# Kernel optimization log

Measured on AMD Instinct MI355X. Metric: run time of the kernel, lower is better.

The kernel has to match this reference:

```python
import jax, jax.numpy as jnp
import numpy as np

B, C, D, H = 2, 512, 512, 8
DH = D // H  # d_head = 64


def setup_inputs() -> dict:
    key = jax.random.key(0)
    ks = jax.random.split(key, 8)
    init = lambda k, shape: 0.02 * jax.random.normal(k, shape, dtype=jnp.float32)
    return {
        "x": jax.random.normal(ks[0], (B, C, D), dtype=jnp.float32),
        "Wq": init(ks[1], (D, D)), "bq": jnp.zeros((D,), jnp.float32),
        "Wk": init(ks[2], (D, D)), "bk": jnp.zeros((D,), jnp.float32),
        "Wv": init(ks[3], (D, D)), "bv": jnp.zeros((D,), jnp.float32),
        "W1": init(ks[4], (3 * DH, DH)), "b1": jnp.zeros((DH,), jnp.float32),
        "W2": init(ks[5], (DH, 1)), "b2": jnp.zeros((1,), jnp.float32),
        "Wo": init(ks[6], (D, D)), "bo": jnp.zeros((D,), jnp.float32),
    }


def reference(x, Wq, bq, Wk, bk, Wv, bv, W1, b1, W2, b2, Wo, bo):
    b, c, dm = x.shape
    # projections -> [B, H, C, d_head]
    q = (x @ Wq + bq).reshape(b, c, H, DH).transpose(0, 2, 1, 3)
    k = (x @ Wk + bk).reshape(b, c, H, DH).transpose(0, 2, 1, 3)
    v = (x @ Wv + bv).reshape(b, c, H, DH).transpose(0, 2, 1, 3)
    # split first MLP weight: [q || k || q*k] @ W1 = q@W1q + k@W1k + (q*k)@W1i
    W1q, W1k, W1i = W1[:DH], W1[DH:2 * DH], W1[2 * DH:]
    hq = jnp.einsum('bhid,de->bhie', q, W1q)   # [B,H,C,d]
    hk = jnp.einsum('bhjd,de->bhje', k, W1k)   # [B,H,C,d]
    hi = jnp.einsum('bhid,bhjd,de->bhije', q, k, W1i)  # [B,H,C,C,d] dominant intermediate
    h = hi + hq[:, :, :, None, :] + hk[:, :, None, :, :] + b1
    g = jax.nn.gelu(h, approximate=False)  # torch nn.GELU is exact erf form
    scores = (jnp.einsum('bhije,e->bhij', g, W2[:, 0]) + b2[0]) / (DH ** 0.5)
    attn = jax.nn.softmax(scores, axis=-1)  # dropout is identity in eval
    out = jnp.einsum('bhij,bhjd->bhid', attn, v)
    out = out.transpose(0, 2, 1, 3).reshape(b, c, dm)
    return out @ Wo + bo
```

## Files before the change

kernel.cpp:

```cpp
#include <hip/hip_runtime.h>
#include <hip/hip_bf16.h>
#include <math.h>

#define BB 2
#define CC 512
#define DD 512
#define HH 8
#define DH 64
#define TI 8

typedef __attribute__((ext_vector_type(8))) short short8;
typedef __attribute__((ext_vector_type(16))) float floatx16;
typedef __attribute__((ext_vector_type(2))) float float2v;
typedef unsigned short u16;

__device__ __forceinline__ float fast_rcp(float x) {
#if __has_builtin(__builtin_amdgcn_rcpf)
    return __builtin_amdgcn_rcpf(x);
#else
    return 1.0f / x;
#endif
}

__device__ __forceinline__ unsigned pk_bf16(float a, float b) {
    __hip_bfloat162 h2 = __float22bfloat162_rn(make_float2(a, b));
    unsigned r;
    __builtin_memcpy(&r, &h2, 4);
    return r;
}

__device__ __forceinline__ short8 mk_short8(unsigned u0, unsigned u1,
                                            unsigned u2, unsigned u3) {
    uint4 u = make_uint4(u0, u1, u2, u3);
    short8 r;
    __builtin_memcpy(&r, &u, 16);
    return r;
}

__device__ __forceinline__ float2v pkfma(float2v a, float2v b, float2v c) {
#if __has_builtin(__builtin_elementwise_fma)
    return __builtin_elementwise_fma(a, b, c);
#else
    float2v r; r[0] = fmaf(a[0], b[0], c[0]); r[1] = fmaf(a[1], b[1], c[1]);
    return r;
#endif
}

__device__ __forceinline__ void split_pack(const float* src, unsigned* hpk, unsigned* lpk) {
    #pragma unroll
    for (int p = 0; p < 4; ++p) {
        float a = src[2 * p], b = src[2 * p + 1];
        unsigned hp = pk_bf16(a, b);
        float la = a - __uint_as_float(hp << 16);
        float lb = b - __uint_as_float(hp & 0xffff0000u);
        hpk[p] = hp;
        lpk[p] = pk_bf16(la, lb);
    }
}

#define GC0 0.3989422804f
#define GC1 (-0.0664903801f)

__device__ __forceinline__ float2v gelu_dot2(float2v h, float2v w2, float2v p) {
    float2v s = h * h;
    float2v q = pkfma(s, float2v{GC1, GC1}, float2v{GC0, GC0});
    float2v t = s * q;
    float2v g = pkfma(h, float2v{0.5f, 0.5f}, t);
    return pkfma(g, w2, p);
}

__global__ __launch_bounds__(256) void prep(
    const float* __restrict__ Wq, const float* __restrict__ Wk,
    const float* __restrict__ Wv, const float* __restrict__ Wo,
    const float* __restrict__ W1, const float* __restrict__ b1,
    const float* __restrict__ bq,
    u16* __restrict__ wth, u16* __restrict__ wtl,
    u16* __restrict__ woh, u16* __restrict__ wol,
    float* __restrict__ b1p)
{
    __shared__ float SH[3 * 64 * 68];
    int j = blockIdx.x, t = threadIdx.x;
    if (j < 256) {
        int mat = j >> 6;
        const float* W = (mat == 0) ? Wq : (mat == 1) ? Wk : (mat == 2) ? Wv : Wo;
        u16* oh = (mat < 3) ? wth + (size_t)mat * 262144 : woh;
        u16* ol = (mat < 3) ? wtl + (size_t)mat * 262144 : wol;
        int tile = j & 63;
        int k0 = (tile >> 3) * 64, n0 = (tile & 7) * 64;
        float (*TT)[68] = (float(*)[68])SH;
        int r = t >> 4, c4 = (t & 15) * 4;
        #pragma unroll
        for (int rr = 0; rr < 4; ++rr) {
            int k = r + rr * 16;
            float4 v = *(const float4*)&W[(size_t)(k0 + k) * 512 + n0 + c4];
            TT[c4 + 0][k] = v.x; TT[c4 + 1][k] = v.y;
            TT[c4 + 2][k] = v.z; TT[c4 + 3][k] = v.w;
        }
        __syncthreads();
        int n = t >> 2, kc = (t & 3) * 16;
        #pragma unroll
        for (int g = 0; g < 2; ++g) {
            unsigned hpk[4], lpk[4];
            split_pack(&TT[n][kc + g * 8], hpk, lpk);
            *(uint4*)&oh[(size_t)(n0 + n) * 512 + k0 + kc + g * 8] =
                make_uint4(hpk[0], hpk[1], hpk[2], hpk[3]);
            *(uint4*)&ol[(size_t)(n0 + n) * 512 + k0 + kc + g * 8] =
                make_uint4(lpk[0], lpk[1], lpk[2], lpk[3]);
        }
    } else if (j < 320) {
        int jj = j - 256;
        int D0 = (jj >> 3) * 64, h = jj & 7;
        float (*WQ)[68]  = (float(*)[68])SH;
        float (*W1Q)[68] = (float(*)[68])(SH + 64 * 68);
        float (*OT)[68]  = (float(*)[68])(SH + 2 * 64 * 68);
        int r = t >> 4, c4 = (t & 15) * 4;
        #pragma unroll
        for (int rr = 0; rr < 4; ++rr) {
            int d = r + rr * 16;
            *(float4*)&WQ[d][c4]  = *(const float4*)&Wq[(size_t)(D0 + d) * 512 + h * 64 + c4];
            *(float4*)&W1Q[d][c4] = *(const float4*)&W1[(size_t)d * 64 + c4];
        }
        __syncthreads();
        int D = t & 63, ec = (t >> 6) * 16;
        float outv[16];
        #pragma unroll
        for (int i = 0; i < 16; ++i) outv[i] = 0.0f;
        for (int d4 = 0; d4 < 16; ++d4) {
            float4 wq4 = *(float4*)&WQ[D][d4 * 4];
            float wqa[4] = {wq4.x, wq4.y, wq4.z, wq4.w};
            #pragma unroll
            for (int dd = 0; dd < 4; ++dd) {
                float wv_ = wqa[dd];
                const float* wrow = &W1Q[d4 * 4 + dd][ec];
                #pragma unroll
                for (int i = 0; i < 16; ++i) outv[i] = fmaf(wv_, wrow[i], outv[i]);
            }
        }
        #pragma unroll
        for (int i = 0; i < 16; ++i) OT[ec + i][D] = outv[i];
        __syncthreads();
        int n = t >> 2, kc = (t & 3) * 16;
        u16* oh3 = wth + (size_t)3 * 262144;
        u16* ol3 = wtl + (size_t)3 * 262144;
        #pragma unroll
        for (int g = 0; g < 2; ++g) {
            unsigned hpk[4], lpk[4];
            split_pack(&OT[n][kc + g * 8], hpk, lpk);
            *(uint4*)&oh3[(size_t)(h * 64 + n) * 512 + D0 + kc + g * 8] =
                make_uint4(hpk[0], hpk[1], hpk[2], hpk[3]);
            *(uint4*)&ol3[(size_t)(h * 64 + n) * 512 + D0 + kc + g * 8] =
                make_uint4(lpk[0], lpk[1], lpk[2], lpk[3]);
        }
    } else {
        for (int n = t; n < 512; n += 256) {
            int h = n >> 6, e = n & 63;
            float s = b1[e];
            for (int d = 0; d < 64; ++d)
                s = fmaf(bq[h * 64 + d], W1[(size_t)d * 64 + e], s);
            b1p[n] = s;
        }
    }
}

__global__ __launch_bounds__(256) void gemm_qkv(
    const float* __restrict__ x,
    const u16* __restrict__ wth, const u16* __restrict__ wtl,
    const float* __restrict__ bq, const float* __restrict__ bk,
    const float* __restrict__ bv, const float* __restrict__ b1p,
    float* __restrict__ qw, float* __restrict__ kw, float* __restrict__ vw,
    float* __restrict__ hqc)
{
    __shared__ u16 Ah[64][64], Al[64][64], Bh[64][64], Bl[64][64];
    int t = threadIdx.x;
    int m0 = blockIdx.x * 64;
    int ny = blockIdx.y;
    int mat = ny >> 3, n0 = (ny & 7) * 64;
    const u16* WH = wth + (size_t)mat * 262144;
    const u16* WL = wtl + (size_t)mat * 262144;
    const float* bias = (mat == 0) ? bq : (mat == 1) ? bk : (mat == 2) ? bv : b1p;
    float* out = (mat == 0) ? qw : (mat == 1) ? kw : (mat == 2) ? vw : hqc;

    int lane = t & 63, w = t >> 6;
    int mrow = (w & 1) * 32, ncol = (w >> 1) * 32;
    int col = lane & 31, half = lane >> 5;
    int sr = t >> 2, skc = (t & 3) * 16;

    floatx16 acc = {0.0f,0.0f,0.0f,0.0f,0.0f,0.0f,0.0f,0.0f,
                    0.0f,0.0f,0.0f,0.0f,0.0f,0.0f,0.0f,0.0f};

    for (int k0 = 0; k0 < 512; k0 += 64) {
        float xa[16];
        const float* xr = &x[(size_t)(m0 + sr) * 512 + k0 + skc];
        *(float4*)&xa[0]  = *(const float4*)&xr[0];
        *(float4*)&xa[4]  = *(const float4*)&xr[4];
        *(float4*)&xa[8]  = *(const float4*)&xr[8];
        *(float4*)&xa[12] = *(const float4*)&xr[12];
        #pragma unroll
        for (int g = 0; g < 2; ++g) {
            unsigned hpk[4], lpk[4];
            split_pack(&xa[g * 8], hpk, lpk);
            int gg = (skc >> 3) + g;
            int sw = (gg ^ (sr & 7)) * 8;
            *(uint4*)&Ah[sr][sw] = make_uint4(hpk[0], hpk[1], hpk[2], hpk[3]);
            *(uint4*)&Al[sr][sw] = make_uint4(lpk[0], lpk[1], lpk[2], lpk[3]);
            *(uint4*)&Bh[sr][sw] = *(const uint4*)&WH[(size_t)(n0 + sr) * 512 + k0 + skc + g * 8];
            *(uint4*)&Bl[sr][sw] = *(const uint4*)&WL[(size_t)(n0 + sr) * 512 + k0 + skc + g * 8];
        }
        __syncthreads();
        int ar = mrow + col, br = ncol + col;
        #pragma unroll
        for (int kk = 0; kk < 4; ++kk) {
            int g8 = kk * 2 + half;
            short8 ah = *(short8*)&Ah[ar][(g8 ^ (ar & 7)) * 8];
            short8 al = *(short8*)&Al[ar][(g8 ^ (ar & 7)) * 8];
            short8 bh = *(short8*)&Bh[br][(g8 ^ (br & 7)) * 8];
            short8 bl = *(short8*)&Bl[br][(g8 ^ (br & 7)) * 8];
            acc = __builtin_amdgcn_mfma_f32_32x32x16_bf16(al, bh, acc, 0, 0, 0);
            acc = __builtin_amdgcn_mfma_f32_32x32x16_bf16(ah, bl, acc, 0, 0, 0);
            acc = __builtin_amdgcn_mfma_f32_32x32x16_bf16(ah, bh, acc, 0, 0, 0);
        }
        __syncthreads();
    }
    int h = n0 >> 6;
    int e = ncol + col;
    float bv_ = bias[n0 + e];
    #pragma unroll
    for (int reg = 0; reg < 16; ++reg) {
        int r = m0 + mrow + (reg & 3) + 8 * (reg >> 2) + 4 * half;
        int b = r >> 9, c = r & 511;
        out[((size_t)(b * HH + h) * CC + c) * DH + e] = acc[reg] + bv_;
    }
}

__global__ __launch_bounds__(256) void gemm_out(
    const float* __restrict__ ow,
    const u16* __restrict__ woh, const u16* __restrict__ wol,
    const float* __restrict__ bo, float* __restrict__ y)
{
    __shared__ u16 Ah[64][64], Al[64][64], Bh[64][64], Bl[64][64];
    int t = threadIdx.x;
    int m0 = blockIdx.x * 64, n0 = blockIdx.y * 64;
    int lane = t & 63, w = t >> 6;
    int mrow = (w & 1) * 32, ncol = (w >> 1) * 32;
    int col = lane & 31, half = lane >> 5;
    int sr = t >> 2, skc = (t & 3) * 16;

    floatx16 acc = {0.0f,0.0f,0.0f,0.0f,0.0f,0.0f,0.0f,0.0f,
                    0.0f,0.0f,0.0f,0.0f,0.0f,0.0f,0.0f,0.0f};
    int r = m0 + sr, b = r >> 9, c = r & 511;

    for (int k0 = 0; k0 < 512; k0 += 64) {
        int hh = k0 >> 6;
        float xa[16];
        const float* arow = &ow[((size_t)(b * HH + hh) * CC + c) * DH + skc];
        *(float4*)&xa[0]  = *(const float4*)&arow[0];
        *(float4*)&xa[4]  = *(const float4*)&arow[4];
        *(float4*)&xa[8]  = *(const float4*)&arow[8];
        *(float4*)&xa[12] = *(const float4*)&arow[12];
        #pragma unroll
        for (int g = 0; g < 2; ++g) {
            unsigned hpk[4], lpk[4];
            split_pack(&xa[g * 8], hpk, lpk);
            int gg = (skc >> 3) + g;
            int sw = (gg ^ (sr & 7)) * 8;
            *(uint4*)&Ah[sr][sw] = make_uint4(hpk[0], hpk[1], hpk[2], hpk[3]);
            *(uint4*)&Al[sr][sw] = make_uint4(lpk[0], lpk[1], lpk[2], lpk[3]);
            *(uint4*)&Bh[sr][sw] = *(const uint4*)&woh[(size_t)(n0 + sr) * 512 + k0 + skc + g * 8];
            *(uint4*)&Bl[sr][sw] = *(const uint4*)&wol[(size_t)(n0 + sr) * 512 + k0 + skc + g * 8];
        }
        __syncthreads();
        int ar = mrow + col, br = ncol + col;
        #pragma unroll
        for (int kk = 0; kk < 4; ++kk) {
            int g8 = kk * 2 + half;
            short8 ah = *(short8*)&Ah[ar][(g8 ^ (ar & 7)) * 8];
            short8 al = *(short8*)&Al[ar][(g8 ^ (ar & 7)) * 8];
            short8 bh = *(short8*)&Bh[br][(g8 ^ (br & 7)) * 8];
            short8 bl = *(short8*)&Bl[br][(g8 ^ (br & 7)) * 8];
            acc = __builtin_amdgcn_mfma_f32_32x32x16_bf16(al, bh, acc, 0, 0, 0);
            acc = __builtin_amdgcn_mfma_f32_32x32x16_bf16(ah, bl, acc, 0, 0, 0);
            acc = __builtin_amdgcn_mfma_f32_32x32x16_bf16(ah, bh, acc, 0, 0, 0);
        }
        __syncthreads();
    }
    float bv_ = bo[n0 + ncol + col];
    #pragma unroll
    for (int reg = 0; reg < 16; ++reg) {
        int r2 = m0 + mrow + (reg & 3) + 8 * (reg >> 2) + 4 * half;
        y[(size_t)r2 * 512 + n0 + ncol + col] = acc[reg] + bv_;
    }
}

__global__ __launch_bounds__(256, 2) void attn2(
    const float* qw, const float* __restrict__ kw,
    const float* __restrict__ vw, const float* __restrict__ hqc,
    const float* __restrict__ W1, const float* __restrict__ W2,
    const float* __restrict__ b2p,
    float* ow)
{
    __shared__ u16 Alds[2][64][64];
    __shared__ u16 sc16[TI][512];

    int t = threadIdx.x;
    int lane = t & 63;
    int w = t >> 6;
    int h = lane >> 5;
    int col = lane & 31;

    int bid = blockIdx.x;
    int bh = ((bid & 7) << 1) | (bid >> 9);
    int i0 = ((bid >> 3) & 63) * TI;

    const float* qb  = qw  + ((size_t)bh * CC + i0) * DH;
    const float* hb  = hqc + ((size_t)bh * CC + i0) * DH;
    const float* kb  = kw  + (size_t)bh * CC * DH;
    const float* vb  = vw  + (size_t)bh * CC * DH;

    float w1i_r[16], w1k_r[16];
    {
        int dbase = w * 16;
        #pragma unroll
        for (int dd = 0; dd < 16; ++dd) {
            w1i_r[dd] = W1[(size_t)(128 + dbase + dd) * 64 + lane];
            w1k_r[dd] = W1[(size_t)(64 + dbase + dd) * 64 + lane];
        }
    }

    short8 bfrag[4][4];
    for (int n = 0; n < 4; ++n) {
        int j = w * 128 + n * 32 + col;
        const float* kr = kb + (size_t)j * 64;
        #pragma unroll
        for (int kk = 0; kk < 4; ++kk) {
            int d = kk * 16 + h * 8;
            float4 k0 = *(const float4*)(kr + d);
            float4 k1 = *(const float4*)(kr + d + 4);
            bfrag[n][kk] = mk_short8(pk_bf16(k0.x, k0.y), pk_bf16(k0.z, k0.w),
                                     pk_bf16(k1.x, k1.y), pk_bf16(k1.z, k1.w));
        }
    }

    float2v w2p[2][8];
    #pragma unroll
    for (int m = 0; m < 2; ++m)
        #pragma unroll
        for (int gq = 0; gq < 8; ++gq) {
            int e = m * 32 + (gq >> 1) * 8 + h * 4 + (gq & 1) * 2;
            w2p[m][gq] = float2v{W2[e], W2[e + 1]};
        }

    #define PRODUCE_A(ii, buf)                                                  \
    {                                                                           \
        int e = lane;                                                           \
        int sw = e & 7;                                                         \
        _Pragma("unroll")                                                       \
        for (int gg = 0; gg < 2; ++gg) {                                        \
            int g8 = w * 2 + gg;                                                \
            const float* qr = qb + (ii) * 64 + g8 * 8;                          \
            float4 q0 = *(const float4*)qr;                                     \
            float4 q1 = *(const float4*)(qr + 4);                               \
            float qv[8] = {q0.x, q0.y, q0.z, q0.w, q1.x, q1.y, q1.z, q1.w};     \
            unsigned int pk[4];                                                 \
            _Pragma("unroll")                                                   \
            for (int p2 = 0; p2 < 4; ++p2) {                                    \
                float a0 = fmaf(qv[2 * p2 + 0], w1i_r[gg * 8 + 2 * p2 + 0],     \
                                w1k_r[gg * 8 + 2 * p2 + 0]);                    \
                float a1 = fmaf(qv[2 * p2 + 1], w1i_r[gg * 8 + 2 * p2 + 1],     \
                                w1k_r[gg * 8 + 2 * p2 + 1]);                    \
                pk[p2] = pk_bf16(a0, a1);                                       \
            }                                                                   \
            *(uint4*)&Alds[buf][e][(g8 ^ sw) * 8] =                             \
                make_uint4(pk[0], pk[1], pk[2], pk[3]);                         \
        }                                                                       \
    }

    PRODUCE_A(0, 0);
    __syncthreads();

    for (int ii = 0; ii < TI; ++ii) {
        int cur = ii & 1;

        short8 afrag[2][4];
        #pragma unroll
        for (int m = 0; m < 2; ++m) {
            int e = m * 32 + col;
            int sw = e & 7;
            #pragma unroll
            for (int kk = 0; kk < 4; ++kk) {
                int g8 = kk * 2 + h;
                afrag[m][kk] = *(short8*)&Alds[cur][e][(g8 ^ sw) * 8];
            }
        }
        floatx16 csx[2];
        #pragma unroll
        for (int m = 0; m < 2; ++m)
            #pragma unroll
            for (int g = 0; g < 4; ++g) {
                float4 c4 = *(const float4*)&hb[ii * 64 + m * 32 + g * 8 + h * 4];
                csx[m][g * 4 + 0] = c4.x; csx[m][g * 4 + 1] = c4.y;
                csx[m][g * 4 + 2] = c4.z; csx[m][g * 4 + 3] = c4.w;
            }

        if (ii + 1 < TI) PRODUCE_A(ii + 1, cur ^ 1);

        #pragma unroll
        for (int n = 0; n < 4; ++n) {
            floatx16 acc[2];
            acc[0] = __builtin_amdgcn_mfma_f32_32x32x16_bf16(
                         afrag[0][0], bfrag[n][0], csx[0], 0, 0, 0);
            acc[1] = __builtin_amdgcn_mfma_f32_32x32x16_bf16(
                         afrag[1][0], bfrag[n][0], csx[1], 0, 0, 0);
            #pragma unroll
            for (int kk = 1; kk < 4; ++kk) {
                acc[0] = __builtin_amdgcn_mfma_f32_32x32x16_bf16(
                             afrag[0][kk], bfrag[n][kk], acc[0], 0, 0, 0);
                acc[1] = __builtin_amdgcn_mfma_f32_32x32x16_bf16(
                             afrag[1][kk], bfrag[n][kk], acc[1], 0, 0, 0);
            }
            float2v p2 = {0.0f, 0.0f};
            #pragma unroll
            for (int m = 0; m < 2; ++m)
                #pragma unroll
                for (int g = 0; g < 4; ++g)
                    #pragma unroll
                    for (int pr = 0; pr < 2; ++pr) {
                        float2v hvv = {acc[m][g * 4 + pr * 2],
                                       acc[m][g * 4 + pr * 2 + 1]};
                        p2 = gelu_dot2(hvv, w2p[m][g * 2 + pr], p2);
                    }
            float p = p2[0] + p2[1];
            p += __shfl_xor(p, 32);
            if (h == 0) sc16[ii][w * 128 + n * 32 + col] = (u16)pk_bf16(p, p);
        }
        __syncthreads();
    }
    #undef PRODUCE_A

    float* attn = (float*)Alds;
    float b2v = b2p[0];
    for (int iirow = w; iirow < TI; iirow += 4) {
        float xv[8];
        float m = -1e30f;
        #pragma unroll
        for (int c = 0; c < 8; ++c) {
            float raw = __uint_as_float((unsigned)sc16[iirow][c * 64 + lane] << 16);
            xv[c] = (raw + b2v) * 0.125f;
            m = fmaxf(m, xv[c]);
        }
        #pragma unroll
        for (int o = 1; o < 64; o <<= 1) m = fmaxf(m, __shfl_xor(m, o));
        float s = 0.0f;
        #pragma unroll
        for (int c = 0; c < 8; ++c) { xv[c] = __expf(xv[c] - m); s += xv[c]; }
        #pragma unroll
        for (int o = 1; o < 64; o <<= 1) s += __shfl_xor(s, o);
        float r = fast_rcp(s);
        #pragma unroll
        for (int c = 0; c < 8; ++c) attn[iirow * 512 + c * 64 + lane] = xv[c] * r;
    }
    __syncthreads();

    {
        float* part = (float*)sc16;
        int e4 = (lane & 15) * 4;
        int ip = lane >> 4;
        int ia = 2 * ip, ib = ia + 1;
        float4 aA = {0.0f, 0.0f, 0.0f, 0.0f};
        float4 aB = {0.0f, 0.0f, 0.0f, 0.0f};
        int jbase = w * 128;
        int jrot = 8 * ip;
        #pragma unroll 4
        for (int jj = 0; jj < 128; ++jj) {
            int j = jbase + ((jj + jrot) & 127);
            float4 v4 = *(const float4*)&vb[(size_t)j * 64 + e4];
            float s0 = attn[ia * 512 + j], s1 = attn[ib * 512 + j];
            aA.x = fmaf(s0, v4.x, aA.x); aA.y = fmaf(s0, v4.y, aA.y);
            aA.z = fmaf(s0, v4.z, aA.z); aA.w = fmaf(s0, v4.w, aA.w);
            aB.x = fmaf(s1, v4.x, aB.x); aB.y = fmaf(s1, v4.y, aB.y);
            aB.z = fmaf(s1, v4.z, aB.z); aB.w = fmaf(s1, v4.w, aB.w);
        }
        *(float4*)&part[(w * 8 + ia) * 64 + e4] = aA;
        *(float4*)&part[(w * 8 + ib) * 64 + e4] = aB;
        __syncthreads();
        for (int idx = t; idx < 512; idx += 256) {
            int i = idx >> 6, e = idx & 63;
            float s = part[(0 + i) * 64 + e] + part[(8 + i) * 64 + e]
                    + part[(16 + i) * 64 + e] + part[(24 + i) * 64 + e];
            ow[((size_t)bh * CC + i0 + i) * DH + e] = s;
        }
    }
}

extern "C" void kernel_launch(void* const* d_in, const int* in_sizes, int n_in,
                              void* d_out, int out_size, void* d_ws, size_t ws_size,
                              hipStream_t stream)
{
    const float* x  = (const float*)d_in[0];
    const float* Wq = (const float*)d_in[1];
    const float* bq = (const float*)d_in[2];
    const float* Wk = (const float*)d_in[3];
    const float* bk = (const float*)d_in[4];
    const float* Wv = (const float*)d_in[5];
    const float* bv = (const float*)d_in[6];
    const float* W1 = (const float*)d_in[7];
    const float* b1 = (const float*)d_in[8];
    const float* W2 = (const float*)d_in[9];
    const float* b2 = (const float*)d_in[10];
    const float* Wo = (const float*)d_in[11];
    const float* bo = (const float*)d_in[12];
    float* y  = (float*)d_out;
    float* ws = (float*)d_ws;

    const size_t SEG = (size_t)BB * HH * CC * DH;
    float* qw  = ws;
    float* kw  = ws + SEG;
    float* vw  = ws + 2 * SEG;
    float* hqc = ws + 3 * SEG;
    u16*   wth = (u16*)(ws + 4 * SEG);
    u16*   wtl = (u16*)(ws + 5 * SEG);
    u16*   woh = (u16*)(ws + 6 * SEG);
    u16*   wol = (u16*)(ws + 6 * SEG + 131072);
    float* b1p = ws + 6 * SEG + 262144;
    float* ow  = qw;

    prep<<<dim3(321), 256, 0, stream>>>(Wq, Wk, Wv, Wo, W1, b1, bq,
                                        wth, wtl, woh, wol, b1p);
    gemm_qkv<<<dim3(16, 32), 256, 0, stream>>>(x, wth, wtl, bq, bk, bv, b1p,
                                               qw, kw, vw, hqc);
    attn2<<<dim3(1024), 256, 0, stream>>>(qw, kw, vw, hqc, W1, W2, b2, ow);
    gemm_out<<<dim3(16, 8), 256, 0, stream>>>(ow, woh, wol, bo, y);
}
```

Baseline: 196.1 us.

## Precompute bf16 A tiles in a separate kernel and drop per-row LDS staging

Adds an a_prod kernel that builds, for every query row, the 64x64 bf16 operand q*W1i + W1k and writes it to workspace. attn2 then loads its MFMA A fragments straight from global memory instead of producing them into double-buffered LDS. Scores are also kept in fp32 in shared memory, which removes the per-row __syncthreads. The aim is to take the A-production ALU work and the barriers out of the attention loop. In exchange it writes and then rereads about 64 MB of intermediate data, adds a launch, and rounds W1 to bf16 before the FMA.

```diff
diff --git a/kernel.cpp b/kernel.cpp
--- a/kernel.cpp
+++ b/kernel.cpp
@@ -291,15 +291,59 @@
     }
 }
 
+__global__ __launch_bounds__(256) void a_prod(
+    const float* __restrict__ qw, const float* __restrict__ W1,
+    u16* __restrict__ aw)
+{
+    __shared__ unsigned w1pk[64][64];
+    int t = threadIdx.x;
+    int b = blockIdx.x;
+    int bh = b >> 5;
+    int ti0 = (b & 31) * 16;
+
+    for (int idx = t; idx < 4096; idx += 256) {
+        int d = idx >> 6, e = idx & 63;
+        w1pk[d][e] = pk_bf16(W1[(size_t)(128 + d) * 64 + e],
+                             W1[(size_t)(64 + d) * 64 + e]);
+    }
+    __syncthreads();
+
+    for (int ii = 0; ii < 16; ++ii) {
+        size_t row = (size_t)bh * CC + ti0 + ii;
+        const float* qr = qw + row * DH;
+        u16* tile = aw + row * 4096;
+        #pragma unroll
+        for (int rep = 0; rep < 2; ++rep) {
+            int group = t + rep * 256;
+            int g8 = group >> 6, e = group & 63;
+            float4 q0 = *(const float4*)(qr + g8 * 8);
+            float4 q1 = *(const float4*)(qr + g8 * 8 + 4);
+            float qv[8] = {q0.x, q0.y, q0.z, q0.w, q1.x, q1.y, q1.z, q1.w};
+            unsigned pk[4];
+            #pragma unroll
+            for (int p2 = 0; p2 < 4; ++p2) {
+                unsigned wp0 = w1pk[g8 * 8 + 2 * p2 + 0][e];
+                unsigned wp1 = w1pk[g8 * 8 + 2 * p2 + 1][e];
+                float a0 = fmaf(qv[2 * p2 + 0], __uint_as_float(wp0 << 16),
+                                __uint_as_float(wp0 & 0xffff0000u));
+                float a1 = fmaf(qv[2 * p2 + 1], __uint_as_float(wp1 << 16),
+                                __uint_as_float(wp1 & 0xffff0000u));
+                pk[p2] = pk_bf16(a0, a1);
+            }
+            *(uint4*)&tile[(size_t)(g8 * 64 + e) * 8] =
+                make_uint4(pk[0], pk[1], pk[2], pk[3]);
+        }
+    }
+}
+
 __global__ __launch_bounds__(256, 2) void attn2(
-    const float* qw, const float* __restrict__ kw,
+    const u16* __restrict__ aw, const float* __restrict__ kw,
     const float* __restrict__ vw, const float* __restrict__ hqc,
-    const float* __restrict__ W1, const float* __restrict__ W2,
-    const float* __restrict__ b2p,
+    const float* __restrict__ W2, const float* __restrict__ b2p,
     float* ow)
 {
-    __shared__ u16 Alds[2][64][64];
-    __shared__ u16 sc16[TI][512];
+    __shared__ float attn[TI][512];
+    __shared__ float part[32][64];
 
     int t = threadIdx.x;
     int lane = t & 63;
@@ -311,20 +355,10 @@
     int bh = ((bid & 7) << 1) | (bid >> 9);
     int i0 = ((bid >> 3) & 63) * TI;
 
-    const float* qb  = qw  + ((size_t)bh * CC + i0) * DH;
     const float* hb  = hqc + ((size_t)bh * CC + i0) * DH;
     const float* kb  = kw  + (size_t)bh * CC * DH;
     const float* vb  = vw  + (size_t)bh * CC * DH;
-
-    float w1i_r[16], w1k_r[16];
-    {
-        int dbase = w * 16;
-        #pragma unroll
-        for (int dd = 0; dd < 16; ++dd) {
-            w1i_r[dd] = W1[(size_t)(128 + dbase + dd) * 64 + lane];
-            w1k_r[dd] = W1[(size_t)(64 + dbase + dd) * 64 + lane];
-        }
-    }
+    const u16*   ab  = aw  + ((size_t)bh * CC + i0) * 4096;
 
     short8 bfrag[4][4];
     for (int n = 0; n < 4; ++n) {
@@ -349,46 +383,16 @@
             w2p[m][gq] = float2v{W2[e], W2[e + 1]};
         }
 
-    #define PRODUCE_A(ii, buf)                                                  \
-    {                                                                           \
-        int e = lane;                                                           \
-        int sw = e & 7;                                                         \
-        _Pragma("unroll")                                                       \
-        for (int gg = 0; gg < 2; ++gg) {                                        \
-            int g8 = w * 2 + gg;                                                \
-            const float* qr = qb + (ii) * 64 + g8 * 8;                          \
-            float4 q0 = *(const float4*)qr;                                     \
-            float4 q1 = *(const float4*)(qr + 4);                               \
-            float qv[8] = {q0.x, q0.y, q0.z, q0.w, q1.x, q1.y, q1.z, q1.w};     \
-            unsigned int pk[4];                                                 \
-            _Pragma("unroll")                                                   \
-            for (int p2 = 0; p2 < 4; ++p2) {                                    \
-                float a0 = fmaf(qv[2 * p2 + 0], w1i_r[gg * 8 + 2 * p2 + 0],     \
-                                w1k_r[gg * 8 + 2 * p2 + 0]);                    \
-                float a1 = fmaf(qv[2 * p2 + 1], w1i_r[gg * 8 + 2 * p2 + 1],     \
-                                w1k_r[gg * 8 + 2 * p2 + 1]);                    \
-                pk[p2] = pk_bf16(a0, a1);                                       \
-            }                                                                   \
-            *(uint4*)&Alds[buf][e][(g8 ^ sw) * 8] =                             \
-                make_uint4(pk[0], pk[1], pk[2], pk[3]);                         \
-        }                                                                       \
-    }
-
-    PRODUCE_A(0, 0);
-    __syncthreads();
-
     for (int ii = 0; ii < TI; ++ii) {
-        int cur = ii & 1;
-
+        const u16* tile = ab + (size_t)ii * 4096;
         short8 afrag[2][4];
         #pragma unroll
         for (int m = 0; m < 2; ++m) {
             int e = m * 32 + col;
-            int sw = e & 7;
             #pragma unroll
             for (int kk = 0; kk < 4; ++kk) {
                 int g8 = kk * 2 + h;
-                afrag[m][kk] = *(short8*)&Alds[cur][e][(g8 ^ sw) * 8];
+                afrag[m][kk] = *(const short8*)&tile[(size_t)(g8 * 64 + e) * 8];
             }
         }
         floatx16 csx[2];
@@ -400,8 +404,6 @@
                 csx[m][g * 4 + 0] = c4.x; csx[m][g * 4 + 1] = c4.y;
                 csx[m][g * 4 + 2] = c4.z; csx[m][g * 4 + 3] = c4.w;
             }
-
-        if (ii + 1 < TI) PRODUCE_A(ii + 1, cur ^ 1);
 
         #pragma unroll
         for (int n = 0; n < 4; ++n) {
@@ -430,21 +432,18 @@
                     }
             float p = p2[0] + p2[1];
             p += __shfl_xor(p, 32);
-            if (h == 0) sc16[ii][w * 128 + n * 32 + col] = (u16)pk_bf16(p, p);
-        }
-        __syncthreads();
-    }
-    #undef PRODUCE_A
-
-    float* attn = (float*)Alds;
+            if (h == 0) attn[ii][w * 128 + n * 32 + col] = p;
+        }
+    }
+    __syncthreads();
+
     float b2v = b2p[0];
     for (int iirow = w; iirow < TI; iirow += 4) {
         float xv[8];
         float m = -1e30f;
         #pragma unroll
         for (int c = 0; c < 8; ++c) {
-            float raw = __uint_as_float((unsigned)sc16[iirow][c * 64 + lane] << 16);
-            xv[c] = (raw + b2v) * 0.125f;
+            xv[c] = (attn[iirow][c * 64 + lane] + b2v) * 0.125f;
             m = fmaxf(m, xv[c]);
         }
         #pragma unroll
@@ -456,12 +455,11 @@
         for (int o = 1; o < 64; o <<= 1) s += __shfl_xor(s, o);
         float r = fast_rcp(s);
         #pragma unroll
-        for (int c = 0; c < 8; ++c) attn[iirow * 512 + c * 64 + lane] = xv[c] * r;
+        for (int c = 0; c < 8; ++c) attn[iirow][c * 64 + lane] = xv[c] * r;
     }
     __syncthreads();
 
     {
-        float* part = (float*)sc16;
         int e4 = (lane & 15) * 4;
         int ip = lane >> 4;
         int ia = 2 * ip, ib = ia + 1;
@@ -473,19 +471,19 @@
         for (int jj = 0; jj < 128; ++jj) {
             int j = jbase + ((jj + jrot) & 127);
             float4 v4 = *(const float4*)&vb[(size_t)j * 64 + e4];
-            float s0 = attn[ia * 512 + j], s1 = attn[ib * 512 + j];
+            float s0 = attn[ia][j], s1 = attn[ib][j];
             aA.x = fmaf(s0, v4.x, aA.x); aA.y = fmaf(s0, v4.y, aA.y);
             aA.z = fmaf(s0, v4.z, aA.z); aA.w = fmaf(s0, v4.w, aA.w);
             aB.x = fmaf(s1, v4.x, aB.x); aB.y = fmaf(s1, v4.y, aB.y);
             aB.z = fmaf(s1, v4.z, aB.z); aB.w = fmaf(s1, v4.w, aB.w);
         }
-        *(float4*)&part[(w * 8 + ia) * 64 + e4] = aA;
-        *(float4*)&part[(w * 8 + ib) * 64 + e4] = aB;
+        *(float4*)&part[w * 8 + ia][e4] = aA;
+        *(float4*)&part[w * 8 + ib][e4] = aB;
         __syncthreads();
         for (int idx = t; idx < 512; idx += 256) {
             int i = idx >> 6, e = idx & 63;
-            float s = part[(0 + i) * 64 + e] + part[(8 + i) * 64 + e]
-                    + part[(16 + i) * 64 + e] + part[(24 + i) * 64 + e];
+            float s = part[0 + i][e] + part[8 + i][e]
+                    + part[16 + i][e] + part[24 + i][e];
             ow[((size_t)bh * CC + i0 + i) * DH + e] = s;
         }
     }
@@ -521,12 +519,14 @@
     u16*   woh = (u16*)(ws + 6 * SEG);
     u16*   wol = (u16*)(ws + 6 * SEG + 131072);
     float* b1p = ws + 6 * SEG + 262144;
+    u16*   aw  = (u16*)(ws + 6 * SEG + 262656);
     float* ow  = qw;
 
     prep<<<dim3(321), 256, 0, stream>>>(Wq, Wk, Wv, Wo, W1, b1, bq,
                                         wth, wtl, woh, wol, b1p);
     gemm_qkv<<<dim3(16, 32), 256, 0, stream>>>(x, wth, wtl, bq, bk, bv, b1p,
                                                qw, kw, vw, hqc);
-    attn2<<<dim3(1024), 256, 0, stream>>>(qw, kw, vw, hqc, W1, W2, b2, ow);
+    a_prod<<<dim3(512), 256, 0, stream>>>(qw, W1, aw);
+    attn2<<<dim3(1024), 256, 0, stream>>>(aw, kw, vw, hqc, W2, b2, ow);
     gemm_out<<<dim3(16, 8), 256, 0, stream>>>(ow, woh, wol, bo, y);
 }
```

Result: slower. 205.2 us (+4.6%).

## Compute attn·V with bf16 MFMA using pre-swizzled V fragments

Applied to the files above, without the earlier changes.

The QKV GEMM now also writes V as bf16 in an MFMA-fragment-friendly layout. The attention kernel replaces its scalar fp32 FMA loop over attn·V with 32x32x16 bf16 MFMAs, padding the 8 query rows to 32. This targets the FMA-bound tail of the attention kernel, at the cost of bf16 precision for attn and V and wasted MFMA rows.

```diff
diff --git a/kernel.cpp b/kernel.cpp
--- a/kernel.cpp
+++ b/kernel.cpp
@@ -168,7 +168,7 @@
     const float* __restrict__ bq, const float* __restrict__ bk,
     const float* __restrict__ bv, const float* __restrict__ b1p,
     float* __restrict__ qw, float* __restrict__ kw, float* __restrict__ vw,
-    float* __restrict__ hqc)
+    float* __restrict__ hqc, u16* __restrict__ vf)
 {
     __shared__ u16 Ah[64][64], Al[64][64], Bh[64][64], Bl[64][64];
     int t = threadIdx.x;
@@ -229,6 +229,17 @@
         int r = m0 + mrow + (reg & 3) + 8 * (reg >> 2) + 4 * half;
         int b = r >> 9, c = r & 511;
         out[((size_t)(b * HH + h) * CC + c) * DH + e] = acc[reg] + bv_;
+    }
+    if (mat == 2) {
+        #pragma unroll
+        for (int reg = 0; reg < 16; ++reg) {
+            int r = m0 + mrow + (reg & 3) + 8 * (reg >> 2) + 4 * half;
+            int b = r >> 9, c = r & 511;
+            int bh2 = b * HH + h;
+            u16 val = (u16)(pk_bf16(acc[reg] + bv_, 0.0f) & 0xffffu);
+            vf[((((size_t)bh2 * 32 + (c >> 4)) * 2 + ((c >> 3) & 1)) * 64 + e) * 8
+               + (c & 7)] = val;
+        }
     }
 }
 
@@ -293,7 +304,7 @@
 
 __global__ __launch_bounds__(256, 2) void attn2(
     const float* qw, const float* __restrict__ kw,
-    const float* __restrict__ vw, const float* __restrict__ hqc,
+    const float* __restrict__ hqc, const u16* __restrict__ vf,
     const float* __restrict__ W1, const float* __restrict__ W2,
     const float* __restrict__ b2p,
     float* ow)
@@ -314,7 +325,7 @@
     const float* qb  = qw  + ((size_t)bh * CC + i0) * DH;
     const float* hb  = hqc + ((size_t)bh * CC + i0) * DH;
     const float* kb  = kw  + (size_t)bh * CC * DH;
-    const float* vb  = vw  + (size_t)bh * CC * DH;
+    const u16*   vfb = vf  + (size_t)bh * 32768;
 
     float w1i_r[16], w1k_r[16];
     {
@@ -462,25 +473,34 @@
 
     {
         float* part = (float*)sc16;
-        int e4 = (lane & 15) * 4;
-        int ip = lane >> 4;
-        int ia = 2 * ip, ib = ia + 1;
-        float4 aA = {0.0f, 0.0f, 0.0f, 0.0f};
-        float4 aB = {0.0f, 0.0f, 0.0f, 0.0f};
-        int jbase = w * 128;
-        int jrot = 8 * ip;
-        #pragma unroll 4
-        for (int jj = 0; jj < 128; ++jj) {
-            int j = jbase + ((jj + jrot) & 127);
-            float4 v4 = *(const float4*)&vb[(size_t)j * 64 + e4];
-            float s0 = attn[ia * 512 + j], s1 = attn[ib * 512 + j];
-            aA.x = fmaf(s0, v4.x, aA.x); aA.y = fmaf(s0, v4.y, aA.y);
-            aA.z = fmaf(s0, v4.z, aA.z); aA.w = fmaf(s0, v4.w, aA.w);
-            aB.x = fmaf(s1, v4.x, aB.x); aB.y = fmaf(s1, v4.y, aB.y);
-            aB.z = fmaf(s1, v4.z, aB.z); aB.w = fmaf(s1, v4.w, aB.w);
-        }
-        *(float4*)&part[(w * 8 + ia) * 64 + e4] = aA;
-        *(float4*)&part[(w * 8 + ib) * 64 + e4] = aB;
+        floatx16 pacc[2];
+        pacc[0] = {0.0f,0.0f,0.0f,0.0f,0.0f,0.0f,0.0f,0.0f,
+                   0.0f,0.0f,0.0f,0.0f,0.0f,0.0f,0.0f,0.0f};
+        pacc[1] = pacc[0];
+        #pragma unroll
+        for (int s = 0; s < 8; ++s) {
+            int jg = w * 8 + s;
+            short8 afr = {0, 0, 0, 0, 0, 0, 0, 0};
+            if (col < TI) {
+                const float* ar = &attn[col * 512 + jg * 16 + h * 8];
+                float4 a0 = *(const float4*)ar;
+                float4 a1 = *(const float4*)(ar + 4);
+                afr = mk_short8(pk_bf16(a0.x, a0.y), pk_bf16(a0.z, a0.w),
+                                pk_bf16(a1.x, a1.y), pk_bf16(a1.z, a1.w));
+            }
+            const u16* vrow = vfb + ((size_t)jg * 2 + h) * 512;
+            short8 b0 = *(const short8*)&vrow[(size_t)(col) * 8];
+            short8 b1 = *(const short8*)&vrow[(size_t)(32 + col) * 8];
+            pacc[0] = __builtin_amdgcn_mfma_f32_32x32x16_bf16(afr, b0, pacc[0], 0, 0, 0);
+            pacc[1] = __builtin_amdgcn_mfma_f32_32x32x16_bf16(afr, b1, pacc[1], 0, 0, 0);
+        }
+        #pragma unroll
+        for (int nt = 0; nt < 2; ++nt)
+            #pragma unroll
+            for (int reg = 0; reg < 4; ++reg) {
+                int i = (reg & 3) + 4 * h;
+                part[(w * 8 + i) * 64 + nt * 32 + col] = pacc[nt][reg];
+            }
         __syncthreads();
         for (int idx = t; idx < 512; idx += 256) {
             int i = idx >> 6, e = idx & 63;
@@ -521,12 +541,13 @@
     u16*   woh = (u16*)(ws + 6 * SEG);
     u16*   wol = (u16*)(ws + 6 * SEG + 131072);
     float* b1p = ws + 6 * SEG + 262144;
+    u16*   vf  = (u16*)(ws + 6 * SEG + 262656);
     float* ow  = qw;
 
     prep<<<dim3(321), 256, 0, stream>>>(Wq, Wk, Wv, Wo, W1, b1, bq,
                                         wth, wtl, woh, wol, b1p);
     gemm_qkv<<<dim3(16, 32), 256, 0, stream>>>(x, wth, wtl, bq, bk, bv, b1p,
-                                               qw, kw, vw, hqc);
-    attn2<<<dim3(1024), 256, 0, stream>>>(qw, kw, vw, hqc, W1, W2, b2, ow);
+                                               qw, kw, vw, hqc, vf);
+    attn2<<<dim3(1024), 256, 0, stream>>>(qw, kw, hqc, vf, W1, W2, b2, ow);
     gemm_out<<<dim3(16, 8), 256, 0, stream>>>(ow, woh, wol, bo, y);
 }
```

After: 184.5 us. -5.9%, faster.
